# Kernel optimization log

Hardware: AMD Instinct MI355X
Metric: run time of the kernel (lower is better)

The kernel has to match this reference:

```python
import jax, jax.numpy as jnp
import numpy as np

B, C, H, W, R = 8, 256, 64, 64, 16


def setup_inputs() -> dict:
    key = jax.random.key(0)
    ks = jax.random.split(key, 14)
    def w(k, shape, fan):
        return (jax.random.normal(k, shape, jnp.float32) / np.sqrt(fan)).astype(jnp.float32)
    return {
        "features_depth": jax.random.normal(ks[0], (B, C, H, W), jnp.float32),
        "features_semseg": jax.random.normal(ks[1], (B, C, H, W), jnp.float32),
        "W0": w(ks[2], (C, 2 * C), 2 * C),          # conv_split0 1x1, [out,in]
        "Wdw": w(ks[3], (C, 1, 3, 3), 9),            # depthwise 3x3, groups=C
        "Wq": w(ks[4], (C, C), C),                   # Linear weights [out,in]
        "Wk": w(ks[5], (C, C), C),
        "Wv": w(ks[6], (C, C), C),
        "Wp": w(ks[7], (C, C), C),
        "bp": jnp.zeros((C,), jnp.float32),
        "Wsplit": w(ks[8], (C, C), C),               # conv_split 1x1
        "se_d_w1": w(ks[9], (C // R, C), C),         # SE squeeze conv1x1 (depth)
        "se_d_w2": w(ks[10], (C, C // R), C // R),
        "se_s_w1": w(ks[11], (C // R, C), C),        # SE squeeze conv1x1 (semseg)
        "se_s_w2": w(ks[12], (C, C // R), C // R),
    }


def _l2norm(a, eps=1e-12):
    n = jnp.linalg.norm(a, axis=-1, keepdims=True)
    return a / jnp.maximum(n, eps)


def _se(x, w1, w2):
    # x: [B,C,H,W]; global avg pool -> 1x1 convs -> sigmoid gate
    p = x.mean(axis=(2, 3))                                  # [B,C]
    h = jax.nn.relu(jnp.einsum('rc,bc->br', w1, p))          # [B,C/R]
    g = jax.nn.sigmoid(jnp.einsum('cr,br->bc', w2, h))       # [B,C]
    return x * g[:, :, None, None]


def reference(features_depth, features_semseg, W0, Wdw, Wq, Wk, Wv, Wp, bp,
              Wsplit, se_d_w1, se_d_w2, se_s_w1, se_s_w2):
    x = jnp.concatenate([features_depth, features_semseg], axis=1)  # [B,2C,H,W]
    x = jnp.einsum('oc,bchw->bohw', W0, x)                          # 1x1 conv
    x = jax.lax.conv_general_dilated(
        x, Wdw, window_strides=(1, 1), padding='SAME',
        dimension_numbers=('NCHW', 'OIHW', 'NCHW'), feature_group_count=C)
    xt = x.transpose(0, 2, 3, 1).reshape(B, H * W, C)               # [B,N,C]
    q = (xt @ Wq.T).transpose(0, 2, 1)                              # [B,C,N]
    k = (xt @ Wk.T).transpose(0, 2, 1)
    v = (xt @ Wv.T).transpose(0, 2, 1)
    q = _l2norm(q)
    k = _l2norm(k)
    attn = jax.nn.softmax(jnp.einsum('bcn,bdn->bcd', k, q), axis=-1)  # [B,C,C]
    y = jnp.einsum('bcd,bdn->bcn', attn, v)                         # [B,C,N]
    y = y.transpose(0, 2, 1)                                        # [B,N,C]
    y = y @ Wp.T + bp                                               # proj
    out_c = y.reshape(B, H, W, C).transpose(0, 3, 1, 2)             # [B,C,H,W]
    out_c = jnp.einsum('oc,bchw->bohw', Wsplit, out_c)              # 1x1 conv
    out_depth = _se(out_c, se_d_w1, se_d_w2) + features_depth
    out_semseg = _se(out_c, se_s_w1, se_s_w2) + features_semseg
    return (out_depth, out_semseg)
```

## Files before the change

kernel.cpp:

```cpp
#include <hip/hip_runtime.h>
#include <cstdint>

#define DEVI __device__ __forceinline__

using fx4 = __attribute__((ext_vector_type(4))) float;
using bf8 = __attribute__((ext_vector_type(8))) __bf16;
using s8v = __attribute__((ext_vector_type(8))) short;
typedef unsigned short u16;
typedef unsigned int u32;

DEVI float b2f(u16 u) { return __builtin_bit_cast(float, (u32)u << 16); }
DEVI u16 f2b(float f) {
  u32 u = __builtin_bit_cast(u32, f);
  return (u16)((u + 0x7fffu + ((u >> 16) & 1u)) >> 16);
}

__global__ __launch_bounds__(256) void wcvt6(const float* s0, u16* d0, int n0,
                                             const float* s1, u16* d1, int n1,
                                             const float* s2, u16* d2, int n2,
                                             const float* s3, u16* d3, int n3,
                                             const float* s4, u16* d4, int n4,
                                             const float* s5, u16* d5, int n5) {
  const float* s; u16* d; int n;
  switch (blockIdx.y) {
    case 0: s = s0; d = d0; n = n0; break;
    case 1: s = s1; d = d1; n = n1; break;
    case 2: s = s2; d = d2; n = n2; break;
    case 3: s = s3; d = d3; n = n3; break;
    case 4: s = s4; d = d4; n = n4; break;
    default: s = s5; d = d5; n = n5; break;
  }
  int i = blockIdx.x * 256 + threadIdx.x;
  if (i < n) d[i] = f2b(s[i]);
}

__global__ void pack_cat(const float* __restrict__ fd, const float* __restrict__ fs,
                         u16* __restrict__ out) {
  __shared__ float t[32][33];
  const int b = blockIdx.z;
  const int n0 = blockIdx.x * 32;
  const int g = blockIdx.y;
  const float* src = (g < 8) ? fd : fs;
  const int c0 = (g & 7) * 32;
  const int ccol0 = g * 32;
  const int tx = threadIdx.x;
  const int ty = threadIdx.y;
  const float* sp = src + ((long)b * 256 + c0) * 4096 + n0;
#pragma unroll
  for (int i = 0; i < 4; ++i) {
    int c = ty + i * 8;
    t[c][tx] = sp[(long)c * 4096 + tx];
  }
  __syncthreads();
  u16* op = out + ((long)b * 4096 + n0) * 512 + ccol0;
#pragma unroll
  for (int i = 0; i < 4; ++i) {
    int r = ty + i * 8;
    op[(long)r * 512 + tx] = f2b(t[tx][r]);
  }
}

template <typename OT, bool BIAS>
__global__ __launch_bounds__(256) void gemm_nt(
    const u16* __restrict__ A, long sA, int lda,
    const u16* __restrict__ B, long sB, int ldb,
    OT* __restrict__ C, long sC, long sCs, int ldc,
    const float* __restrict__ bias, int Keff, int ksplit) {
  __shared__ u16 ldsA[128 * 64];
  __shared__ u16 ldsB[128 * 64];
  const int z = blockIdx.z;
  const int bb = z / ksplit;
  const int ss = z - bb * ksplit;
  const int bm = blockIdx.x * 128;
  const int bn = blockIdx.y * 128;
  const u16* Ab = A + bb * sA + (long)ss * Keff;
  const u16* Bb = B + bb * sB + (long)ss * Keff;
  const int tid = threadIdx.x;
  const int wid = tid >> 6;
  const int lane = tid & 63;
  const int wm = wid >> 1, wn = wid & 1;
  const int r8 = lane >> 3, ch = lane & 7;

  fx4 acc[4][4] = {};
  for (int kt = 0; kt < Keff; kt += 64) {
    s8v ga[4], gb[4];
#pragma unroll
    for (int i = 0; i < 4; ++i) {
      const int row = wid * 32 + i * 8 + r8;
      ga[i] = *(const s8v*)&Ab[(long)(bm + row) * lda + kt + ch * 8];
      gb[i] = *(const s8v*)&Bb[(long)(bn + row) * ldb + kt + ch * 8];
    }
#pragma unroll
    for (int i = 0; i < 4; ++i) {
      const int row = wid * 32 + i * 8 + r8;
      const int sw = ((ch ^ (row & 7)) * 8);
      *(s8v*)&ldsA[row * 64 + sw] = ga[i];
      *(s8v*)&ldsB[row * 64 + sw] = gb[i];
    }
    __syncthreads();
#pragma unroll
    for (int ko = 0; ko < 2; ++ko) {
      bf8 af[4], bfr[4];
      const int kq = ko * 4 + (lane >> 4);
#pragma unroll
      for (int f = 0; f < 4; ++f) {
        const int ar = wm * 64 + f * 16 + (lane & 15);
        af[f] = *(const bf8*)&ldsA[ar * 64 + ((kq ^ (ar & 7)) * 8)];
        const int br = wn * 64 + f * 16 + (lane & 15);
        bfr[f] = *(const bf8*)&ldsB[br * 64 + ((kq ^ (br & 7)) * 8)];
      }
#pragma unroll
      for (int fm = 0; fm < 4; ++fm)
#pragma unroll
        for (int fn = 0; fn < 4; ++fn)
          acc[fm][fn] = __builtin_amdgcn_mfma_f32_16x16x32_bf16(af[fm], bfr[fn], acc[fm][fn], 0, 0, 0);
    }
    __syncthreads();
  }
  OT* Cb = C + bb * sC + ss * sCs;
#pragma unroll
  for (int fm = 0; fm < 4; ++fm) {
    const int m0 = bm + wm * 64 + fm * 16 + ((lane >> 4) << 2);
#pragma unroll
    for (int fn = 0; fn < 4; ++fn) {
      const int n0 = bn + wn * 64 + fn * 16 + (lane & 15);
      float bv = 0.f;
      if (BIAS) bv = bias[n0];
#pragma unroll
      for (int r = 0; r < 4; ++r) {
        float v = acc[fm][fn][r] + bv;
        if constexpr (sizeof(OT) == 2) Cb[(long)(m0 + r) * ldc + n0] = (OT)f2b(v);
        else Cb[(long)(m0 + r) * ldc + n0] = v;
      }
    }
  }
}

__global__ __launch_bounds__(256) void dwconv3x3(const u16* __restrict__ x,
                                                 const float* __restrict__ wdw,
                                                 u16* __restrict__ y) {
  __shared__ float w[9][256];
  const int t = threadIdx.x;
  for (int i = t; i < 2304; i += 256) w[i % 9][i / 9] = wdw[i];
  __syncthreads();
  const int nb = blockIdx.x;
  const int b = nb >> 9;
  const int n0 = (nb & 511) << 3;
  const int tn = t >> 5;
  const int tc = (t & 31) << 3;
  const int n = n0 + tn;
  const int hh = n >> 6, ww2 = n & 63;
  const u16* base = x + ((long)b << 20);
  float acc[8] = {0.f, 0.f, 0.f, 0.f, 0.f, 0.f, 0.f, 0.f};
#pragma unroll
  for (int ky = 0; ky < 3; ++ky) {
    const int hy = hh + ky - 1;
    if ((unsigned)hy >= 64u) continue;
#pragma unroll
    for (int kx = 0; kx < 3; ++kx) {
      const int wx = ww2 + kx - 1;
      if ((unsigned)wx >= 64u) continue;
      const s8v v = *(const s8v*)&base[(((hy << 6) + wx) << 8) + tc];
      const int kk = ky * 3 + kx;
      const fx4 wa = *(const fx4*)&w[kk][tc];
      const fx4 wb = *(const fx4*)&w[kk][tc + 4];
#pragma unroll
      for (int j = 0; j < 4; ++j) {
        acc[j] += wa[j] * b2f((u16)v[j]);
        acc[4 + j] += wb[j] * b2f((u16)v[4 + j]);
      }
    }
  }
  s8v o;
#pragma unroll
  for (int j = 0; j < 8; ++j) o[j] = (short)f2b(acc[j]);
  *(s8v*)&y[((long)b << 20) + ((long)n << 8) + tc] = o;
}

__global__ __launch_bounds__(256) void l2norm_rows(u16* __restrict__ buf) {
  const long row = blockIdx.x;
  u16* p = buf + row * 4096;
  const int t = threadIdx.x;
  s8v a = ((s8v*)p)[t * 2];
  s8v b = ((s8v*)p)[t * 2 + 1];
  float ss = 0.f;
#pragma unroll
  for (int j = 0; j < 8; ++j) {
    float xa = b2f((u16)a[j]); ss += xa * xa;
    float xb = b2f((u16)b[j]); ss += xb * xb;
  }
#pragma unroll
  for (int o = 32; o > 0; o >>= 1) ss += __shfl_xor(ss, o);
  __shared__ float red[4];
  if ((t & 63) == 0) red[t >> 6] = ss;
  __syncthreads();
  const float tot = red[0] + red[1] + red[2] + red[3];
  const float sc = 1.f / fmaxf(sqrtf(tot), 1e-12f);
#pragma unroll
  for (int j = 0; j < 8; ++j) {
    a[j] = (short)f2b(b2f((u16)a[j]) * sc);
    b[j] = (short)f2b(b2f((u16)b[j]) * sc);
  }
  ((s8v*)p)[t * 2] = a;
  ((s8v*)p)[t * 2 + 1] = b;
}

__global__ __launch_bounds__(256) void softmax_splits(const float* __restrict__ part,
                                                      u16* __restrict__ out,
                                                      int nsplit, long sstride) {
  const int wid = threadIdx.x >> 6, lane = threadIdx.x & 63;
  const long row = (long)blockIdx.x * 4 + wid;
  fx4 v = {0.f, 0.f, 0.f, 0.f};
  for (int s = 0; s < nsplit; ++s)
    v += ((const fx4*)(part + s * sstride + row * 256))[lane];
  float m = fmaxf(fmaxf(v[0], v[1]), fmaxf(v[2], v[3]));
#pragma unroll
  for (int o = 32; o > 0; o >>= 1) m = fmaxf(m, __shfl_xor(m, o));
  float e0 = __expf(v[0] - m), e1 = __expf(v[1] - m);
  float e2 = __expf(v[2] - m), e3 = __expf(v[3] - m);
  float s4 = e0 + e1 + e2 + e3;
#pragma unroll
  for (int o = 32; o > 0; o >>= 1) s4 += __shfl_xor(s4, o);
  const float inv = 1.f / s4;
  u16* op = out + row * 256 + lane * 4;
  op[0] = f2b(e0 * inv); op[1] = f2b(e1 * inv);
  op[2] = f2b(e2 * inv); op[3] = f2b(e3 * inv);
}

__global__ __launch_bounds__(256) void rowmean(const float* __restrict__ x, float* __restrict__ pooled) {
  const long row = blockIdx.x;
  const fx4* p = (const fx4*)(x + row * 4096);
  const int t = threadIdx.x;
  float s = 0.f;
#pragma unroll
  for (int i = 0; i < 4; ++i) {
    fx4 v = p[t * 4 + i];
    s += v[0] + v[1] + v[2] + v[3];
  }
#pragma unroll
  for (int o = 32; o > 0; o >>= 1) s += __shfl_xor(s, o);
  __shared__ float red[4];
  if ((t & 63) == 0) red[t >> 6] = s;
  __syncthreads();
  if (t == 0) pooled[row] = (red[0] + red[1] + red[2] + red[3]) * (1.f / 4096.f);
}

__global__ __launch_bounds__(256) void se_gates(const float* __restrict__ pooled,
                                                const float* __restrict__ w1d, const float* __restrict__ w2d,
                                                const float* __restrict__ w1s, const float* __restrict__ w2s,
                                                float* __restrict__ gd, float* __restrict__ gs) {
  const int b = blockIdx.x;
  const int t = threadIdx.x;
  __shared__ float p[256], hd[16], hs[16];
  p[t] = pooled[b * 256 + t];
  __syncthreads();
  if (t < 16) {
    float ad = 0.f, as2 = 0.f;
    for (int j = 0; j < 256; ++j) {
      ad += w1d[t * 256 + j] * p[j];
      as2 += w1s[t * 256 + j] * p[j];
    }
    hd[t] = fmaxf(ad, 0.f);
    hs[t] = fmaxf(as2, 0.f);
  }
  __syncthreads();
  float ad = 0.f, as2 = 0.f;
#pragma unroll
  for (int r = 0; r < 16; ++r) {
    ad += w2d[t * 16 + r] * hd[r];
    as2 += w2s[t * 16 + r] * hs[r];
  }
  gd[b * 256 + t] = 1.f / (1.f + __expf(-ad));
  gs[b * 256 + t] = 1.f / (1.f + __expf(-as2));
}

__global__ __launch_bounds__(256) void fuse_out(const float* __restrict__ oc,
                                                const float* __restrict__ gd, const float* __restrict__ gs,
                                                const float* __restrict__ fd, const float* __restrict__ fs,
                                                float* __restrict__ od, float* __restrict__ os) {
  const long i = ((long)blockIdx.x * 256 + threadIdx.x) * 4;
  const long bc = i >> 12;
  const float gdv = gd[bc], gsv = gs[bc];
  const fx4 c = *(const fx4*)(oc + i);
  const fx4 a = *(const fx4*)(fd + i);
  const fx4 s = *(const fx4*)(fs + i);
  *(fx4*)(od + i) = c * gdv + a;
  *(fx4*)(os + i) = c * gsv + s;
}

extern "C" void kernel_launch(void* const* d_in, const int* in_sizes, int n_in,
                              void* d_out, int out_size, void* d_ws, size_t ws_size,
                              hipStream_t stream) {
  const float* fd  = (const float*)d_in[0];
  const float* fs  = (const float*)d_in[1];
  const float* W0  = (const float*)d_in[2];
  const float* Wdw = (const float*)d_in[3];
  const float* Wq  = (const float*)d_in[4];
  const float* Wk  = (const float*)d_in[5];
  const float* Wv  = (const float*)d_in[6];
  const float* Wp  = (const float*)d_in[7];
  const float* bp  = (const float*)d_in[8];
  const float* Wsp = (const float*)d_in[9];
  const float* w1d = (const float*)d_in[10];
  const float* w2d = (const float*)d_in[11];
  const float* w1s = (const float*)d_in[12];
  const float* w2s = (const float*)d_in[13];

  char* ws = (char*)d_ws;
  u16* catb  = (u16*)(ws + 0);
  u16* qb    = (u16*)(ws + 0);
  u16* kb    = (u16*)(ws + 16777216);
  u16* x0b   = (u16*)(ws + 33554432);
  u16* ytb   = x0b;
  u16* xtb   = (u16*)(ws + 50331648);
  u16* zb    = xtb;
  u16* vtb   = (u16*)(ws + 67108864);
  u16* asmb  = (u16*)(ws + 83886080);
  float* outc = (float*)(ws + 84934656);
  float* part = outc;
  u16* w0b = (u16*)(ws + 118489088);
  u16* wqb = w0b + 131072;
  u16* wkb = wqb + 65536;
  u16* wvb = wkb + 65536;
  u16* wpb = wvb + 65536;
  u16* wsb = wpb + 65536;
  float* pooled = (float*)(ws + 119406592);
  float* gdp    = (float*)(ws + 119414784);
  float* gsp    = (float*)(ws + 119422976);
  float* od  = (float*)d_out;
  float* osg = od + 8388608;

  wcvt6<<<dim3(512, 6), 256, 0, stream>>>(W0, w0b, 131072, Wq, wqb, 65536, Wk, wkb, 65536,
                                          Wv, wvb, 65536, Wp, wpb, 65536, Wsp, wsb, 65536);
  pack_cat<<<dim3(128, 16, 8), dim3(32, 8), 0, stream>>>(fd, fs, catb);
  gemm_nt<u16, false><<<dim3(32, 2, 8), 256, 0, stream>>>(catb, 2097152, 512, w0b, 0, 512,
                                                          x0b, 1048576, 0, 256, nullptr, 512, 1);
  dwconv3x3<<<4096, 256, 0, stream>>>(x0b, Wdw, xtb);
  gemm_nt<u16, false><<<dim3(2, 32, 8), 256, 0, stream>>>(wqb, 0, 256, xtb, 1048576, 256,
                                                          qb, 1048576, 0, 4096, nullptr, 256, 1);
  gemm_nt<u16, false><<<dim3(2, 32, 8), 256, 0, stream>>>(wkb, 0, 256, xtb, 1048576, 256,
                                                          kb, 1048576, 0, 4096, nullptr, 256, 1);
  gemm_nt<u16, false><<<dim3(32, 2, 8), 256, 0, stream>>>(xtb, 1048576, 256, wvb, 0, 256,
                                                          vtb, 1048576, 0, 256, nullptr, 256, 1);
  l2norm_rows<<<2048, 256, 0, stream>>>(qb);
  l2norm_rows<<<2048, 256, 0, stream>>>(kb);
  gemm_nt<float, false><<<dim3(2, 2, 64), 256, 0, stream>>>(kb, 1048576, 4096, qb, 1048576, 4096,
                                                            part, 65536, 524288, 256, nullptr, 512, 8);
  softmax_splits<<<512, 256, 0, stream>>>(part, asmb, 8, 524288);
  gemm_nt<u16, false><<<dim3(32, 2, 8), 256, 0, stream>>>(vtb, 1048576, 256, asmb, 65536, 256,
                                                          ytb, 1048576, 0, 256, nullptr, 256, 1);
  gemm_nt<u16, true><<<dim3(32, 2, 8), 256, 0, stream>>>(ytb, 1048576, 256, wpb, 0, 256,
                                                         zb, 1048576, 0, 256, bp, 256, 1);
  gemm_nt<float, false><<<dim3(2, 32, 8), 256, 0, stream>>>(wsb, 0, 256, zb, 1048576, 256,
                                                            outc, 1048576, 0, 4096, nullptr, 256, 1);
  rowmean<<<2048, 256, 0, stream>>>(outc, pooled);
  se_gates<<<8, 256, 0, stream>>>(pooled, w1d, w2d, w1s, w2s, gdp, gsp);
  fuse_out<<<8192, 256, 0, stream>>>(outc, gdp, gsp, fd, fs, od, osg);
}
```

Baseline: 199.7 us.

## Fold proj into split conv, fuse Q/K GEMM, defer L2 norm, pool in epilogue

Precomputes Wsplit·Wp and its bias so the projection and split 1x1 conv become one GEMM, and merges the Q and K GEMMs into a single launch. The L2 normalisation is no longer applied in place: row inverse norms are computed separately and applied inside the softmax. The SE average pool is folded into the final GEMM epilogue through partial sums, so the separate rowmean kernel is removed. The final GEMM now writes bf16 instead of fp32, which halves the traffic into fuse_out. GEMM tile loads switch to direct global-to-LDS loads. In exchange there is an extra small weight-product kernel, and the pooled mean is taken from fp32 values before they are rounded to bf16.

```diff
diff --git a/kernel.cpp b/kernel.cpp
--- a/kernel.cpp
+++ b/kernel.cpp
@@ -15,23 +15,44 @@
   return (u16)((u + 0x7fffu + ((u >> 16) & 1u)) >> 16);
 }
 
-__global__ __launch_bounds__(256) void wcvt6(const float* s0, u16* d0, int n0,
-                                             const float* s1, u16* d1, int n1,
-                                             const float* s2, u16* d2, int n2,
-                                             const float* s3, u16* d3, int n3,
-                                             const float* s4, u16* d4, int n4,
-                                             const float* s5, u16* d5, int n5) {
+#define GLOAD(g, l)                                                          \
+  __builtin_amdgcn_global_load_lds(                                          \
+      (const __attribute__((address_space(1))) unsigned int*)(g),            \
+      (__attribute__((address_space(3))) unsigned int*)(l), 16, 0, 0)
+
+__global__ __launch_bounds__(256) void wcvt(const float* s0, u16* d0, int n0,
+                                            const float* s1, u16* d1, int n1,
+                                            const float* s2, u16* d2, int n2,
+                                            const float* s3, u16* d3, int n3) {
   const float* s; u16* d; int n;
   switch (blockIdx.y) {
     case 0: s = s0; d = d0; n = n0; break;
     case 1: s = s1; d = d1; n = n1; break;
     case 2: s = s2; d = d2; n = n2; break;
-    case 3: s = s3; d = d3; n = n3; break;
-    case 4: s = s4; d = d4; n = n4; break;
-    default: s = s5; d = d5; n = n5; break;
+    default: s = s3; d = d3; n = n3; break;
   }
   int i = blockIdx.x * 256 + threadIdx.x;
   if (i < n) d[i] = f2b(s[i]);
+}
+
+__global__ __launch_bounds__(256) void wcmul(const float* __restrict__ Wsp,
+                                             const float* __restrict__ Wp,
+                                             const float* __restrict__ bp,
+                                             u16* __restrict__ wcb, float* __restrict__ bc) {
+  const int o = blockIdx.x, t = threadIdx.x;
+  __shared__ float row[256];
+  __shared__ float red[4];
+  row[t] = Wsp[o * 256 + t];
+  __syncthreads();
+  float acc = 0.f;
+  for (int c = 0; c < 256; ++c) acc += row[c] * Wp[c * 256 + t];
+  wcb[o * 256 + t] = f2b(acc);
+  float pb = row[t] * bp[t];
+#pragma unroll
+  for (int m = 32; m > 0; m >>= 1) pb += __shfl_xor(pb, m);
+  if ((t & 63) == 0) red[t >> 6] = pb;
+  __syncthreads();
+  if (t == 0) bc[o] = red[0] + red[1] + red[2] + red[3];
 }
 
 __global__ void pack_cat(const float* __restrict__ fd, const float* __restrict__ fs,
@@ -60,12 +81,13 @@
   }
 }
 
-template <typename OT, bool BIAS>
+template <typename OT, int BIAS, bool POOL>
 __global__ __launch_bounds__(256) void gemm_nt(
     const u16* __restrict__ A, long sA, int lda,
     const u16* __restrict__ B, long sB, int ldb,
     OT* __restrict__ C, long sC, long sCs, int ldc,
-    const float* __restrict__ bias, int Keff, int ksplit) {
+    const float* __restrict__ bias, int Keff, int ksplit,
+    float* __restrict__ poolpart) {
   __shared__ u16 ldsA[128 * 64];
   __shared__ u16 ldsB[128 * 64];
   const int z = blockIdx.z;
@@ -73,29 +95,23 @@
   const int ss = z - bb * ksplit;
   const int bm = blockIdx.x * 128;
   const int bn = blockIdx.y * 128;
-  const u16* Ab = A + bb * sA + (long)ss * Keff;
-  const u16* Bb = B + bb * sB + (long)ss * Keff;
+  const u16* Ab = A + bb * sA + (long)ss * Keff + (long)bm * lda;
+  const u16* Bb = B + bb * sB + (long)ss * Keff + (long)bn * ldb;
   const int tid = threadIdx.x;
   const int wid = tid >> 6;
   const int lane = tid & 63;
   const int wm = wid >> 1, wn = wid & 1;
-  const int r8 = lane >> 3, ch = lane & 7;
+  const int srow = tid >> 3;
+  const int slot = tid & 7;
 
   fx4 acc[4][4] = {};
   for (int kt = 0; kt < Keff; kt += 64) {
-    s8v ga[4], gb[4];
 #pragma unroll
     for (int i = 0; i < 4; ++i) {
-      const int row = wid * 32 + i * 8 + r8;
-      ga[i] = *(const s8v*)&Ab[(long)(bm + row) * lda + kt + ch * 8];
-      gb[i] = *(const s8v*)&Bb[(long)(bn + row) * ldb + kt + ch * 8];
-    }
-#pragma unroll
-    for (int i = 0; i < 4; ++i) {
-      const int row = wid * 32 + i * 8 + r8;
-      const int sw = ((ch ^ (row & 7)) * 8);
-      *(s8v*)&ldsA[row * 64 + sw] = ga[i];
-      *(s8v*)&ldsB[row * 64 + sw] = gb[i];
+      const int row = i * 32 + srow;
+      const int kq = slot ^ (row & 7);
+      GLOAD(Ab + (long)row * lda + kt + kq * 8, &ldsA[i * 2048 + wid * 512]);
+      GLOAD(Bb + (long)row * ldb + kt + kq * 8, &ldsB[i * 2048 + wid * 512]);
     }
     __syncthreads();
 #pragma unroll
@@ -118,21 +134,43 @@
     __syncthreads();
   }
   OT* Cb = C + bb * sC + ss * sCs;
+  float pr[4][4];
+  if (POOL) {
+#pragma unroll
+    for (int fm = 0; fm < 4; ++fm)
+#pragma unroll
+      for (int r = 0; r < 4; ++r) pr[fm][r] = 0.f;
+  }
 #pragma unroll
   for (int fm = 0; fm < 4; ++fm) {
     const int m0 = bm + wm * 64 + fm * 16 + ((lane >> 4) << 2);
 #pragma unroll
     for (int fn = 0; fn < 4; ++fn) {
       const int n0 = bn + wn * 64 + fn * 16 + (lane & 15);
-      float bv = 0.f;
-      if (BIAS) bv = bias[n0];
+      float bvn = (BIAS == 1) ? bias[n0] : 0.f;
 #pragma unroll
       for (int r = 0; r < 4; ++r) {
-        float v = acc[fm][fn][r] + bv;
+        float v = acc[fm][fn][r] + bvn;
+        if (BIAS == 2) v += bias[m0 + r];
         if constexpr (sizeof(OT) == 2) Cb[(long)(m0 + r) * ldc + n0] = (OT)f2b(v);
         else Cb[(long)(m0 + r) * ldc + n0] = v;
+        if (POOL) pr[fm][r] += v;
       }
     }
+  }
+  if (POOL) {
+#pragma unroll
+    for (int fm = 0; fm < 4; ++fm)
+#pragma unroll
+      for (int r = 0; r < 4; ++r) {
+        float s = pr[fm][r];
+        s += __shfl_xor(s, 1); s += __shfl_xor(s, 2);
+        s += __shfl_xor(s, 4); s += __shfl_xor(s, 8);
+        if ((lane & 15) == 0) {
+          const int o = bm + wm * 64 + fm * 16 + ((lane >> 4) << 2) + r;
+          poolpart[(long)(blockIdx.y * 2 + wn) * 2048 + bb * 256 + o] = s;
+        }
+      }
   }
 }
 
@@ -177,42 +215,40 @@
   *(s8v*)&y[((long)b << 20) + ((long)n << 8) + tc] = o;
 }
 
-__global__ __launch_bounds__(256) void l2norm_rows(u16* __restrict__ buf) {
+__global__ __launch_bounds__(256) void rownorm(const u16* __restrict__ qk,
+                                               float* __restrict__ rinv) {
   const long row = blockIdx.x;
-  u16* p = buf + row * 4096;
+  const u16* p = qk + row * 4096;
   const int t = threadIdx.x;
-  s8v a = ((s8v*)p)[t * 2];
-  s8v b = ((s8v*)p)[t * 2 + 1];
   float ss = 0.f;
 #pragma unroll
-  for (int j = 0; j < 8; ++j) {
-    float xa = b2f((u16)a[j]); ss += xa * xa;
-    float xb = b2f((u16)b[j]); ss += xb * xb;
+  for (int c = 0; c < 2; ++c) {
+    s8v a = ((const s8v*)p)[t * 2 + c];
+#pragma unroll
+    for (int j = 0; j < 8; ++j) { float x = b2f((u16)a[j]); ss += x * x; }
   }
 #pragma unroll
   for (int o = 32; o > 0; o >>= 1) ss += __shfl_xor(ss, o);
   __shared__ float red[4];
   if ((t & 63) == 0) red[t >> 6] = ss;
   __syncthreads();
-  const float tot = red[0] + red[1] + red[2] + red[3];
-  const float sc = 1.f / fmaxf(sqrtf(tot), 1e-12f);
-#pragma unroll
-  for (int j = 0; j < 8; ++j) {
-    a[j] = (short)f2b(b2f((u16)a[j]) * sc);
-    b[j] = (short)f2b(b2f((u16)b[j]) * sc);
-  }
-  ((s8v*)p)[t * 2] = a;
-  ((s8v*)p)[t * 2 + 1] = b;
+  if (t == 0) rinv[row] = 1.f / fmaxf(sqrtf(red[0] + red[1] + red[2] + red[3]), 1e-12f);
 }
 
 __global__ __launch_bounds__(256) void softmax_splits(const float* __restrict__ part,
-                                                      u16* __restrict__ out,
-                                                      int nsplit, long sstride) {
+                                                      const float* __restrict__ rinv,
+                                                      u16* __restrict__ out) {
   const int wid = threadIdx.x >> 6, lane = threadIdx.x & 63;
   const long row = (long)blockIdx.x * 4 + wid;
+  const int b = (int)(row >> 8);
+  const int c = (int)(row & 255);
   fx4 v = {0.f, 0.f, 0.f, 0.f};
-  for (int s = 0; s < nsplit; ++s)
-    v += ((const fx4*)(part + s * sstride + row * 256))[lane];
+#pragma unroll
+  for (int s = 0; s < 8; ++s)
+    v += ((const fx4*)(part + s * 524288 + row * 256))[lane];
+  const float rk = rinv[b * 512 + 256 + c];
+  const fx4 rq = *(const fx4*)&rinv[b * 512 + lane * 4];
+  v[0] *= rk * rq[0]; v[1] *= rk * rq[1]; v[2] *= rk * rq[2]; v[3] *= rk * rq[3];
   float m = fmaxf(fmaxf(v[0], v[1]), fmaxf(v[2], v[3]));
 #pragma unroll
   for (int o = 32; o > 0; o >>= 1) m = fmaxf(m, __shfl_xor(m, o));
@@ -227,32 +263,17 @@
   op[2] = f2b(e2 * inv); op[3] = f2b(e3 * inv);
 }
 
-__global__ __launch_bounds__(256) void rowmean(const float* __restrict__ x, float* __restrict__ pooled) {
-  const long row = blockIdx.x;
-  const fx4* p = (const fx4*)(x + row * 4096);
-  const int t = threadIdx.x;
-  float s = 0.f;
-#pragma unroll
-  for (int i = 0; i < 4; ++i) {
-    fx4 v = p[t * 4 + i];
-    s += v[0] + v[1] + v[2] + v[3];
-  }
-#pragma unroll
-  for (int o = 32; o > 0; o >>= 1) s += __shfl_xor(s, o);
-  __shared__ float red[4];
-  if ((t & 63) == 0) red[t >> 6] = s;
-  __syncthreads();
-  if (t == 0) pooled[row] = (red[0] + red[1] + red[2] + red[3]) * (1.f / 4096.f);
-}
-
-__global__ __launch_bounds__(256) void se_gates(const float* __restrict__ pooled,
+__global__ __launch_bounds__(256) void se_gates(const float* __restrict__ poolpart,
                                                 const float* __restrict__ w1d, const float* __restrict__ w2d,
                                                 const float* __restrict__ w1s, const float* __restrict__ w2s,
                                                 float* __restrict__ gd, float* __restrict__ gs) {
   const int b = blockIdx.x;
   const int t = threadIdx.x;
   __shared__ float p[256], hd[16], hs[16];
-  p[t] = pooled[b * 256 + t];
+  float s = 0.f;
+#pragma unroll 8
+  for (int sl = 0; sl < 64; ++sl) s += poolpart[(long)sl * 2048 + b * 256 + t];
+  p[t] = s * (1.f / 4096.f);
   __syncthreads();
   if (t < 16) {
     float ad = 0.f, as2 = 0.f;
@@ -274,18 +295,26 @@
   gs[b * 256 + t] = 1.f / (1.f + __expf(-as2));
 }
 
-__global__ __launch_bounds__(256) void fuse_out(const float* __restrict__ oc,
+__global__ __launch_bounds__(256) void fuse_out(const u16* __restrict__ oc,
                                                 const float* __restrict__ gd, const float* __restrict__ gs,
                                                 const float* __restrict__ fd, const float* __restrict__ fs,
                                                 float* __restrict__ od, float* __restrict__ os) {
-  const long i = ((long)blockIdx.x * 256 + threadIdx.x) * 4;
+  const long i = ((long)blockIdx.x * 256 + threadIdx.x) * 8;
   const long bc = i >> 12;
   const float gdv = gd[bc], gsv = gs[bc];
-  const fx4 c = *(const fx4*)(oc + i);
-  const fx4 a = *(const fx4*)(fd + i);
-  const fx4 s = *(const fx4*)(fs + i);
-  *(fx4*)(od + i) = c * gdv + a;
-  *(fx4*)(os + i) = c * gsv + s;
+  const s8v c8 = *(const s8v*)&oc[i];
+  const fx4 a0 = *(const fx4*)(fd + i), a1 = *(const fx4*)(fd + i + 4);
+  const fx4 s0 = *(const fx4*)(fs + i), s1 = *(const fx4*)(fs + i + 4);
+  fx4 d0, d1, e0, e1;
+#pragma unroll
+  for (int j = 0; j < 4; ++j) {
+    const float cl = b2f((u16)c8[j]);
+    const float ch = b2f((u16)c8[4 + j]);
+    d0[j] = cl * gdv + a0[j]; d1[j] = ch * gdv + a1[j];
+    e0[j] = cl * gsv + s0[j]; e1[j] = ch * gsv + s1[j];
+  }
+  *(fx4*)(od + i) = d0; *(fx4*)(od + i + 4) = d1;
+  *(fx4*)(os + i) = e0; *(fx4*)(os + i + 4) = e1;
 }
 
 extern "C" void kernel_launch(void* const* d_in, const int* in_sizes, int n_in,
@@ -307,53 +336,47 @@
   const float* w2s = (const float*)d_in[13];
 
   char* ws = (char*)d_ws;
-  u16* catb  = (u16*)(ws + 0);
-  u16* qb    = (u16*)(ws + 0);
-  u16* kb    = (u16*)(ws + 16777216);
-  u16* x0b   = (u16*)(ws + 33554432);
-  u16* ytb   = x0b;
-  u16* xtb   = (u16*)(ws + 50331648);
-  u16* zb    = xtb;
-  u16* vtb   = (u16*)(ws + 67108864);
-  u16* asmb  = (u16*)(ws + 83886080);
-  float* outc = (float*)(ws + 84934656);
-  float* part = outc;
-  u16* w0b = (u16*)(ws + 118489088);
-  u16* wqb = w0b + 131072;
-  u16* wkb = wqb + 65536;
-  u16* wvb = wkb + 65536;
-  u16* wpb = wvb + 65536;
-  u16* wsb = wpb + 65536;
-  float* pooled = (float*)(ws + 119406592);
-  float* gdp    = (float*)(ws + 119414784);
-  float* gsp    = (float*)(ws + 119422976);
+  u16* catb   = (u16*)(ws + 0);
+  u16* qkb    = catb;
+  u16* x0b    = (u16*)(ws + 33554432);
+  u16* ytb    = x0b;
+  u16* xtb    = (u16*)(ws + 50331648);
+  u16* outcb  = xtb;
+  u16* vtb    = (u16*)(ws + 67108864);
+  u16* asmb   = (u16*)(ws + 83886080);
+  float* part = (float*)(ws + 84934656);
+  u16* w0b    = (u16*)(ws + 101711872);
+  u16* wqkb   = (u16*)(ws + 101974016);
+  u16* wvb    = (u16*)(ws + 102236160);
+  u16* wcb    = (u16*)(ws + 102367232);
+  float* bcb  = (float*)(ws + 102498304);
+  float* rinv = (float*)(ws + 102499328);
+  float* poolpart = (float*)(ws + 102515712);
+  float* gdp  = (float*)(ws + 103040000);
+  float* gsp  = (float*)(ws + 103048192);
   float* od  = (float*)d_out;
   float* osg = od + 8388608;
 
-  wcvt6<<<dim3(512, 6), 256, 0, stream>>>(W0, w0b, 131072, Wq, wqb, 65536, Wk, wkb, 65536,
-                                          Wv, wvb, 65536, Wp, wpb, 65536, Wsp, wsb, 65536);
+  wcvt<<<dim3(512, 4), 256, 0, stream>>>(W0, w0b, 131072, Wq, wqkb, 65536,
+                                         Wk, wqkb + 65536, 65536, Wv, wvb, 65536);
+  wcmul<<<256, 256, 0, stream>>>(Wsp, Wp, bp, wcb, bcb);
   pack_cat<<<dim3(128, 16, 8), dim3(32, 8), 0, stream>>>(fd, fs, catb);
-  gemm_nt<u16, false><<<dim3(32, 2, 8), 256, 0, stream>>>(catb, 2097152, 512, w0b, 0, 512,
-                                                          x0b, 1048576, 0, 256, nullptr, 512, 1);
+  gemm_nt<u16, 0, false><<<dim3(32, 2, 8), 256, 0, stream>>>(
+      catb, 2097152, 512, w0b, 0, 512, x0b, 1048576, 0, 256, nullptr, 512, 1, nullptr);
   dwconv3x3<<<4096, 256, 0, stream>>>(x0b, Wdw, xtb);
-  gemm_nt<u16, false><<<dim3(2, 32, 8), 256, 0, stream>>>(wqb, 0, 256, xtb, 1048576, 256,
-                                                          qb, 1048576, 0, 4096, nullptr, 256, 1);
-  gemm_nt<u16, false><<<dim3(2, 32, 8), 256, 0, stream>>>(wkb, 0, 256, xtb, 1048576, 256,
-                                                          kb, 1048576, 0, 4096, nullptr, 256, 1);
-  gemm_nt<u16, false><<<dim3(32, 2, 8), 256, 0, stream>>>(xtb, 1048576, 256, wvb, 0, 256,
-                                                          vtb, 1048576, 0, 256, nullptr, 256, 1);
-  l2norm_rows<<<2048, 256, 0, stream>>>(qb);
-  l2norm_rows<<<2048, 256, 0, stream>>>(kb);
-  gemm_nt<float, false><<<dim3(2, 2, 64), 256, 0, stream>>>(kb, 1048576, 4096, qb, 1048576, 4096,
-                                                            part, 65536, 524288, 256, nullptr, 512, 8);
-  softmax_splits<<<512, 256, 0, stream>>>(part, asmb, 8, 524288);
-  gemm_nt<u16, false><<<dim3(32, 2, 8), 256, 0, stream>>>(vtb, 1048576, 256, asmb, 65536, 256,
-                                                          ytb, 1048576, 0, 256, nullptr, 256, 1);
-  gemm_nt<u16, true><<<dim3(32, 2, 8), 256, 0, stream>>>(ytb, 1048576, 256, wpb, 0, 256,
-                                                         zb, 1048576, 0, 256, bp, 256, 1);
-  gemm_nt<float, false><<<dim3(2, 32, 8), 256, 0, stream>>>(wsb, 0, 256, zb, 1048576, 256,
-                                                            outc, 1048576, 0, 4096, nullptr, 256, 1);
-  rowmean<<<2048, 256, 0, stream>>>(outc, pooled);
-  se_gates<<<8, 256, 0, stream>>>(pooled, w1d, w2d, w1s, w2s, gdp, gsp);
-  fuse_out<<<8192, 256, 0, stream>>>(outc, gdp, gsp, fd, fs, od, osg);
-}
+  gemm_nt<u16, 0, false><<<dim3(4, 32, 8), 256, 0, stream>>>(
+      wqkb, 0, 256, xtb, 1048576, 256, qkb, 2097152, 0, 4096, nullptr, 256, 1, nullptr);
+  gemm_nt<u16, 0, false><<<dim3(32, 2, 8), 256, 0, stream>>>(
+      xtb, 1048576, 256, wvb, 0, 256, vtb, 1048576, 0, 256, nullptr, 256, 1, nullptr);
+  rownorm<<<4096, 256, 0, stream>>>(qkb, rinv);
+  gemm_nt<float, 0, false><<<dim3(2, 2, 64), 256, 0, stream>>>(
+      qkb + 1048576, 2097152, 4096, qkb, 2097152, 4096,
+      part, 65536, 524288, 256, nullptr, 512, 8, nullptr);
+  softmax_splits<<<512, 256, 0, stream>>>(part, rinv, asmb);
+  gemm_nt<u16, 0, false><<<dim3(32, 2, 8), 256, 0, stream>>>(
+      vtb, 1048576, 256, asmb, 65536, 256, ytb, 1048576, 0, 256, nullptr, 256, 1, nullptr);
+  gemm_nt<u16, 2, true><<<dim3(2, 32, 8), 256, 0, stream>>>(
+      wcb, 0, 256, ytb, 1048576, 256, outcb, 1048576, 0, 4096, bcb, 256, 1, poolpart);
+  se_gates<<<8, 256, 0, stream>>>(poolpart, w1d, w2d, w1s, w2s, gdp, gsp);
+  fuse_out<<<4096, 256, 0, stream>>>(outcb, gdp, gsp, fd, fs, od, osg);
+}
```

New measurement: 179.4 us. 1.11x faster.
